# Kernel tuning notes

Hardware: AMD Instinct MI355X
Metric: run time of the kernel (lower is better)

The kernel has to match this reference:

```python
import jax, jax.numpy as jnp
import numpy as np

T, N, E = 512, 64, 1024   # encoder frames, batch, encoder feature dim
H = 320                   # pred_hidden_size
J = 512                   # joint hidden
V = 29                    # vocab incl. blank
BLANK = V - 1
MAX_SYM = 30              # max_symbols_per_step


def setup_inputs() -> dict:
    key = jax.random.key(0)
    ks = jax.random.split(key, 16)
    sH = 1.0 / np.sqrt(H)
    sE = 1.0 / np.sqrt(E)
    sJ = 1.0 / np.sqrt(J)
    b_o = jax.random.normal(ks[14], (V,), jnp.float32) * 0.1
    b_o = b_o.at[BLANK].add(4.0)  # blank-dominant logits -> realistic sparse emissions
    return {
        "f": jax.random.normal(ks[0], (T, N, E), jnp.float32),
        "f_lens": jax.random.randint(ks[1], (N,), T // 2, T + 1).astype(jnp.int32),
        "emb": jax.random.normal(ks[2], (V - 1, H), jnp.float32) * 0.1,
        "wi0": jax.random.normal(ks[3], (4 * H, H), jnp.float32) * sH,
        "wh0": jax.random.normal(ks[4], (4 * H, H), jnp.float32) * sH,
        "bi0": jax.random.normal(ks[5], (4 * H,), jnp.float32) * 0.05,
        "bh0": jax.random.normal(ks[6], (4 * H,), jnp.float32) * 0.05,
        "wi1": jax.random.normal(ks[7], (4 * H, H), jnp.float32) * sH,
        "wh1": jax.random.normal(ks[8], (4 * H, H), jnp.float32) * sH,
        "bi1": jax.random.normal(ks[9], (4 * H,), jnp.float32) * 0.05,
        "bh1": jax.random.normal(ks[10], (4 * H,), jnp.float32) * 0.05,
        "w_f": jax.random.normal(ks[11], (J, E), jnp.float32) * sE,
        "w_g": jax.random.normal(ks[12], (J, H), jnp.float32) * sH,
        "b_j": jax.random.normal(ks[13], (J,), jnp.float32) * 0.05,
        "w_o": jax.random.normal(ks[15], (V, J), jnp.float32) * sJ,
        "b_o": b_o,
    }


def reference(f, f_lens, emb, wi0, wh0, bi0, bh0, wi1, wh1, bi1, bh1,
              w_f, w_g, b_j, w_o, b_o):
    n = f.shape[1]
    rows = jnp.arange(n)

    def cell(x, h, c, wi, wh, bi, bh):
        g = x @ wi.T + h @ wh.T + (bi + bh)
        i, fg, gg, o = jnp.split(g, 4, axis=-1)  # torch LSTM gate order i,f,g,o
        c2 = jax.nn.sigmoid(fg) * c + jax.nn.sigmoid(i) * jnp.tanh(gg)
        return jax.nn.sigmoid(o) * jnp.tanh(c2), c2

    def pred_step(last_sym, h, c):
        # SOS (=-1) embeds to zeros
        x = jnp.where(last_sym[:, None] < 0, 0.0, emb[jnp.clip(last_sym, 0, V - 2)])
        h0, c0 = cell(x, h[0], c[0], wi0, wh0, bi0, bh0)
        h1, c1 = cell(h0, h[1], c[1], wi1, wh1, bi1, bh1)
        return h1, jnp.stack([h0, h1]), jnp.stack([c0, c1])

    def joint(fi, g):
        hj = jax.nn.relu(fi @ w_f.T + g @ w_g.T + b_j)
        return hj @ w_o.T + b_o

    def cond(st):
        return jnp.any(st[0] < f_lens)

    def body(st):
        time_idx, sym_add, res, res_idx, last, h, c = st
        fi = f[jnp.clip(time_idx, 0, T - 1), rows]            # [N,E] per-element frame
        g, h_new, c_new = pred_step(last, h, c)               # one LSTM step
        sym = jnp.argmax(joint(fi, g), axis=1).astype(jnp.int32)
        active = time_idx < f_lens
        emit = active & (sym != BLANK) & (sym_add < MAX_SYM)
        adv = active & ~emit                                   # blank or symbol cap -> advance time
        slot = jnp.where(emit, res_idx + 1, 0)
        res = res.at[rows, slot].set(jnp.where(emit, sym, res[rows, slot]))
        res_idx = res_idx + emit.astype(jnp.int32)
        sym_add = jnp.where(emit, sym_add + 1, jnp.where(adv, 0, sym_add))
        time_idx = time_idx + adv.astype(jnp.int32)
        last = jnp.where(emit, sym, last)
        m = emit[None, :, None]
        return (time_idx, sym_add, res, res_idx, last,
                jnp.where(m, h_new, h), jnp.where(m, c_new, c))

    init = (jnp.zeros((n,), jnp.int32),                        # time_idx
            jnp.zeros((n,), jnp.int32),                        # symbols_added
            jnp.full((n, MAX_SYM * T), -1, jnp.int32),         # res
            jnp.full((n,), -1, jnp.int32),                     # res_idx
            jnp.full((n,), -1, jnp.int32),                     # pred_g (SOS)
            jnp.zeros((2, n, H), jnp.float32),                 # pred h
            jnp.zeros((2, n, H), jnp.float32))                 # pred c
    st = jax.lax.while_loop(cond, body, init)
    res, res_idx = st[2], st[3]
    return res, res_idx + 1
```

## Files before the change

kernel.cpp:

```cpp
#include <hip/hip_runtime.h>
#include <math.h>

#define T_ 512
#define N_ 64
#define E_ 1024
#define H_ 320
#define HS8_ 40
#define J_ 512
#define V_ 29
#define BLANK_ 28
#define MAXSYM_ 30
#define RESW_ (MAXSYM_ * T_)

#define BM_ 128
#define BN_ 128
#define BK_ 16
#define GEMMB_ 1024

__device__ float g_Xi0[V_][4 * H_];
__device__ float g_b1s[4 * H_];
__device__ float g_h0x[2][N_][H_];
__device__ float g_h1x[2][N_][H_];
__device__ float g_gpx[2][N_][8][J_];
__device__ unsigned int g_flag[N_];

#define BSW_ 144
__device__ __forceinline__ int padcol(int c) { return c + ((c >> 5) << 2); }

__global__ __launch_bounds__(256) void gemm_init_kernel(
    const float* __restrict__ A, const float* __restrict__ B,
    const float* __restrict__ bj, float* __restrict__ C,
    const float* __restrict__ emb, const float* __restrict__ wi0,
    const float* __restrict__ bi0, const float* __restrict__ bh0,
    const float* __restrict__ bi1, const float* __restrict__ bh1,
    int* __restrict__ res) {
  const int bid = blockIdx.x;
  const int tid = threadIdx.x;

  if (bid >= GEMMB_) {
    const int ab = bid - GEMMB_;
    if (ab < V_) {
      __shared__ __align__(16) float xs[H_];
      for (int i = tid; i < H_; i += 256)
        xs[i] = (ab < V_ - 1) ? emb[(size_t)ab * H_ + i] : 0.f;
      __syncthreads();
      for (int o = tid; o < 4 * H_; o += 256) {
        float acc = bi0[o] + bh0[o];
        if (ab < V_ - 1) {
          const float* wr = wi0 + (size_t)o * H_;
          for (int k = 0; k < H_; k += 4) {
            float4 x4 = *(const float4*)&xs[k];
            float4 w4 = *(const float4*)&wr[k];
            acc += x4.x * w4.x + x4.y * w4.y + x4.z * w4.z + x4.w * w4.w;
          }
        }
        g_Xi0[ab][o] = acc;
        if (ab == 0) g_b1s[o] = bi1[o] + bh1[o];
      }
    } else {
      if (ab == V_ && tid < N_) g_flag[tid] = 0u;
      const int fb = ab - V_;
      int4* r4 = (int4*)res;
      const size_t tot = (size_t)N_ * RESW_ / 4;
      const size_t i0 = (size_t)fb * 256 + tid;
      const int4 mval = {-1, -1, -1, -1};
      for (size_t i = i0; i < tot; i += 3 * 256) r4[i] = mval;
    }
    return;
  }

  __shared__ __align__(16) float As[BK_][BM_ + 4];
  __shared__ __align__(16) float Bs[BK_][BSW_];
  const int m0 = blockIdx.x / 4 * BM_;
  const int j0 = (blockIdx.x & 3) * BN_;
  const int tx = tid & 15, ty = tid >> 4;
  const int sm = tid >> 1;
  const int sk = (tid & 1) << 3;
  const int smP = padcol(sm);
  const int bcol = padcol(tx * 8);

  float acc[8][8];
#pragma unroll
  for (int i = 0; i < 8; ++i)
#pragma unroll
    for (int j = 0; j < 8; ++j) acc[i][j] = 0.f;

  for (int kc = 0; kc < E_; kc += BK_) {
    float4 av0 = *(const float4*)(A + (size_t)(m0 + sm) * E_ + kc + sk);
    float4 av1 = *(const float4*)(A + (size_t)(m0 + sm) * E_ + kc + sk + 4);
    float4 bv0 = *(const float4*)(B + (size_t)(j0 + sm) * E_ + kc + sk);
    float4 bv1 = *(const float4*)(B + (size_t)(j0 + sm) * E_ + kc + sk + 4);
    __syncthreads();
    As[sk + 0][sm] = av0.x; As[sk + 1][sm] = av0.y;
    As[sk + 2][sm] = av0.z; As[sk + 3][sm] = av0.w;
    As[sk + 4][sm] = av1.x; As[sk + 5][sm] = av1.y;
    As[sk + 6][sm] = av1.z; As[sk + 7][sm] = av1.w;
    Bs[sk + 0][smP] = bv0.x; Bs[sk + 1][smP] = bv0.y;
    Bs[sk + 2][smP] = bv0.z; Bs[sk + 3][smP] = bv0.w;
    Bs[sk + 4][smP] = bv1.x; Bs[sk + 5][smP] = bv1.y;
    Bs[sk + 6][smP] = bv1.z; Bs[sk + 7][smP] = bv1.w;
    __syncthreads();
#pragma unroll
    for (int k = 0; k < BK_; ++k) {
      float a_[8], b_[8];
      *(float4*)&a_[0] = *(const float4*)&As[k][ty * 8];
      *(float4*)&a_[4] = *(const float4*)&As[k][ty * 8 + 4];
      *(float4*)&b_[0] = *(const float4*)&Bs[k][bcol];
      *(float4*)&b_[4] = *(const float4*)&Bs[k][bcol + 4];
#pragma unroll
      for (int i = 0; i < 8; ++i)
#pragma unroll
        for (int j = 0; j < 8; ++j) acc[i][j] += a_[i] * b_[j];
    }
  }

#pragma unroll
  for (int i = 0; i < 8; ++i) {
    const size_t m = (size_t)(m0 + ty * 8 + i);
#pragma unroll
    for (int j = 0; j < 8; j += 4) {
      float4 v;
      v.x = acc[i][j + 0] + bj[j0 + tx * 8 + j + 0];
      v.y = acc[i][j + 1] + bj[j0 + tx * 8 + j + 1];
      v.z = acc[i][j + 2] + bj[j0 + tx * 8 + j + 2];
      v.w = acc[i][j + 3] + bj[j0 + tx * 8 + j + 3];
      *(float4*)(C + m * J_ + j0 + tx * 8 + j) = v;
    }
  }
}

__device__ __forceinline__ float sigmoidf_(float x) {
  return 1.f / (1.f + expf(-x));
}

__device__ __forceinline__ void flag_round8(int row, int tid, int& target) {
  target += 8;
  __syncthreads();
  if (tid == 0) {
    __hip_atomic_fetch_add(&g_flag[row], 1u, __ATOMIC_RELEASE,
                           __HIP_MEMORY_SCOPE_AGENT);
    while (__hip_atomic_load(&g_flag[row], __ATOMIC_ACQUIRE,
                             __HIP_MEMORY_SCOPE_AGENT) < (unsigned)target)
      __builtin_amdgcn_s_sleep(1);
  }
  __syncthreads();
}

__device__ void recompute8(
    int s, int row, int k8, int tid, int par, int& target,
    const float* __restrict__ wh0, const float* __restrict__ wi1,
    const float* __restrict__ wh1, const float* __restrict__ w_g,
    float* h0s, float* h1s, float* gates,
    float& c0, float& c1, float2& gp) {
  const int g = tid / HS8_;
  const int il = tid - g * HS8_;
  const int o = g * H_ + k8 * HS8_ + il;

  if (tid < 4 * HS8_) {
    const float* wr = wh0 + (size_t)o * H_;
    float acc = g_Xi0[s][o];
    for (int kk = 0; kk < H_; kk += 4) {
      float4 h4 = *(const float4*)&h0s[kk];
      float4 w4 = *(const float4*)&wr[kk];
      acc += h4.x * w4.x + h4.y * w4.y + h4.z * w4.z + h4.w * w4.w;
    }
    gates[tid] = acc;
  }
  __syncthreads();
  if (tid < HS8_) {
    float ig = sigmoidf_(gates[tid]);
    float fg = sigmoidf_(gates[HS8_ + tid]);
    float gg = tanhf(gates[2 * HS8_ + tid]);
    float og = sigmoidf_(gates[3 * HS8_ + tid]);
    float c2 = fg * c0 + ig * gg;
    c0 = c2;
    float h2 = og * tanhf(c2);
    __hip_atomic_store(&g_h0x[par][row][k8 * HS8_ + tid], h2, __ATOMIC_RELAXED,
                       __HIP_MEMORY_SCOPE_AGENT);
  }
  float acc1 = 0.f;
  if (tid < 4 * HS8_) {
    const float* whr = wh1 + (size_t)o * H_;
    acc1 = g_b1s[o];
    for (int kk = 0; kk < H_; kk += 4) {
      float4 h4 = *(const float4*)&h1s[kk];
      float4 w4 = *(const float4*)&whr[kk];
      acc1 += h4.x * w4.x + h4.y * w4.y + h4.z * w4.z + h4.w * w4.w;
    }
  }
  flag_round8(row, tid, target);
  h0s[tid] = __hip_atomic_load(&g_h0x[par][row][tid], __ATOMIC_RELAXED,
                               __HIP_MEMORY_SCOPE_AGENT);
  if (tid < H_ - 256)
    h0s[256 + tid] = __hip_atomic_load(&g_h0x[par][row][256 + tid],
                                       __ATOMIC_RELAXED, __HIP_MEMORY_SCOPE_AGENT);
  __syncthreads();
  if (tid < 4 * HS8_) {
    const float* wir = wi1 + (size_t)o * H_;
    for (int kk = 0; kk < H_; kk += 4) {
      float4 x4 = *(const float4*)&h0s[kk];
      float4 w4 = *(const float4*)&wir[kk];
      acc1 += x4.x * w4.x + x4.y * w4.y + x4.z * w4.z + x4.w * w4.w;
    }
    gates[tid] = acc1;
  }
  __syncthreads();
  if (tid < HS8_) {
    float ig = sigmoidf_(gates[tid]);
    float fg = sigmoidf_(gates[HS8_ + tid]);
    float gg = tanhf(gates[2 * HS8_ + tid]);
    float og = sigmoidf_(gates[3 * HS8_ + tid]);
    float c2 = fg * c1 + ig * gg;
    c1 = c2;
    float h2 = og * tanhf(c2);
    h1s[k8 * HS8_ + tid] = h2;
    __hip_atomic_store(&g_h1x[par][row][k8 * HS8_ + tid], h2, __ATOMIC_RELAXED,
                       __HIP_MEMORY_SCOPE_AGENT);
  }
  __syncthreads();
  {
    const float* hsl = &h1s[k8 * HS8_];
#pragma unroll
    for (int jj = 0; jj < 2; ++jj) {
      const int j = tid + jj * 256;
      const float* wgr = w_g + (size_t)j * H_ + k8 * HS8_;
      float a = 0.f;
      for (int kk = 0; kk < HS8_; kk += 4) {
        float4 h4 = *(const float4*)&hsl[kk];
        float4 w4 = *(const float4*)&wgr[kk];
        a += h4.x * w4.x + h4.y * w4.y + h4.z * w4.z + h4.w * w4.w;
      }
      __hip_atomic_store(&g_gpx[par][row][k8][j], a, __ATOMIC_RELAXED,
                         __HIP_MEMORY_SCOPE_AGENT);
    }
  }
  flag_round8(row, tid, target);
  {
    float ax = 0.f, ay = 0.f;
#pragma unroll
    for (int kk = 0; kk < 8; ++kk) {
      ax += __hip_atomic_load(&g_gpx[par][row][kk][2 * tid], __ATOMIC_RELAXED,
                              __HIP_MEMORY_SCOPE_AGENT);
      ay += __hip_atomic_load(&g_gpx[par][row][kk][2 * tid + 1], __ATOMIC_RELAXED,
                              __HIP_MEMORY_SCOPE_AGENT);
    }
    gp.x = ax; gp.y = ay;
  }
  h1s[tid] = __hip_atomic_load(&g_h1x[par][row][tid], __ATOMIC_RELAXED,
                               __HIP_MEMORY_SCOPE_AGENT);
  if (tid < H_ - 256)
    h1s[256 + tid] = __hip_atomic_load(&g_h1x[par][row][256 + tid],
                                       __ATOMIC_RELAXED, __HIP_MEMORY_SCOPE_AGENT);
  __syncthreads();
}

__global__ __launch_bounds__(256, 2) void decode8(
    const float* __restrict__ Fproj, const int* __restrict__ f_lens,
    const float* __restrict__ wh0,
    const float* __restrict__ wi1, const float* __restrict__ wh1,
    const float* __restrict__ w_g,
    const float* __restrict__ w_o, const float* __restrict__ b_o,
    int* __restrict__ res, int* __restrict__ nsym) {
  const int bid = blockIdx.x;
  const int k8 = bid & 7;
  const int row = ((bid >> 3) + 8 * k8) & 63;
  const int tid = threadIdx.x;
  const int f_len = f_lens[row];

  __shared__ __align__(16) float h0s[H_], h1s[H_];
  __shared__ __align__(16) float gates[4 * HS8_];
  __shared__ __align__(16) float hjs[J_];
  __shared__ float logits[32];

  const int v = tid >> 3;
  const int lq = tid & 7;
  float4 wo[16];
  float bo = 0.f;
  if (v < V_) {
#pragma unroll
    for (int q = 0; q < 16; ++q)
      wo[q] = *(const float4*)(w_o + (size_t)v * J_ + lq * 4 + 32 * q);
    bo = b_o[v];
  }

  for (int i = tid; i < H_; i += 256) { h0s[i] = 0.f; h1s[i] = 0.f; }
  float c0 = 0.f, c1 = 0.f;
  float2 gp = {0.f, 0.f};
  int target = 0;
  __syncthreads();

  recompute8(BLANK_, row, k8, tid, 0, target, wh0, wi1, wh1, w_g,
             h0s, h1s, gates, c0, c1, gp);
  int ecount = 1;

  int t_loc = 0, sym_add = 0, res_idx = -1;
  float2 fp = *(const float2*)(Fproj + (size_t)row * J_ + 2 * tid);

  while (t_loc < f_len) {
    const int tn = (t_loc + 1 < T_) ? t_loc + 1 : T_ - 1;
    float2 fpn = *(const float2*)(Fproj + ((size_t)tn * N_ + row) * J_ + 2 * tid);

    float hx = fp.x + gp.x, hy = fp.y + gp.y;
    float2 hj2 = {hx > 0.f ? hx : 0.f, hy > 0.f ? hy : 0.f};
    *(float2*)&hjs[2 * tid] = hj2;
    __syncthreads();

    float p = 0.f;
    if (v < V_) {
#pragma unroll
      for (int q = 0; q < 16; ++q) {
        float4 h4 = *(const float4*)&hjs[lq * 4 + 32 * q];
        p += h4.x * wo[q].x + h4.y * wo[q].y + h4.z * wo[q].z + h4.w * wo[q].w;
      }
    }
    p += __shfl_xor(p, 4, 8);
    p += __shfl_xor(p, 2, 8);
    p += __shfl_xor(p, 1, 8);
    if (v < V_ && lq == 0) logits[v] = p + bo;
    __syncthreads();

    float best = logits[0];
    int bi = 0;
#pragma unroll
    for (int vv = 1; vv < V_; ++vv) {
      float lv = logits[vv];
      if (lv > best) { best = lv; bi = vv; }
    }
    const int emit = (bi != BLANK_) && (sym_add < MAXSYM_);

    if (emit) {
      res_idx += 1;
      if (k8 == 0 && tid == 0) res[(size_t)row * RESW_ + res_idx] = bi;
      sym_add += 1;
      recompute8(bi, row, k8, tid, ecount & 1, target, wh0, wi1, wh1, w_g,
                 h0s, h1s, gates, c0, c1, gp);
      ecount += 1;
    } else {
      sym_add = 0;
      t_loc += 1;
      fp = fpn;
    }
  }

  if (k8 == 0 && tid == 0) nsym[row] = res_idx + 1;
}

extern "C" void kernel_launch(void* const* d_in, const int* in_sizes, int n_in,
                              void* d_out, int out_size, void* d_ws, size_t ws_size,
                              hipStream_t stream) {
  const float* f      = (const float*)d_in[0];
  const int*   f_lens = (const int*)d_in[1];
  const float* emb    = (const float*)d_in[2];
  const float* wi0    = (const float*)d_in[3];
  const float* wh0    = (const float*)d_in[4];
  const float* bi0    = (const float*)d_in[5];
  const float* bh0    = (const float*)d_in[6];
  const float* wi1    = (const float*)d_in[7];
  const float* wh1    = (const float*)d_in[8];
  const float* bi1    = (const float*)d_in[9];
  const float* bh1    = (const float*)d_in[10];
  const float* w_f    = (const float*)d_in[11];
  const float* w_g    = (const float*)d_in[12];
  const float* b_j    = (const float*)d_in[13];
  const float* w_o    = (const float*)d_in[14];
  const float* b_o    = (const float*)d_in[15];

  int* out  = (int*)d_out;
  int* res  = out;
  int* nsym = out + (size_t)N_ * RESW_;

  float* Fproj = (float*)d_ws;

  gemm_init_kernel<<<GEMMB_ + 32, 256, 0, stream>>>(
      f, w_f, b_j, Fproj, emb, wi0, bi0, bh0, bi1, bh1, res);

  decode8<<<N_ * 8, 256, 0, stream>>>(Fproj, f_lens, wh0, wi1, wh1, w_g,
                                      w_o, b_o, res, nsym);
}
```

Baseline: 1.932 ms.

## Split each decode row across 16 cooperating blocks with split-K gate dot products

The per-row decode is spread over 16 blocks instead of 8. Each block now owns 20 hidden units, and two threads split each gate row's K dimension and combine their halves with a shuffle. This cuts the serial dot-product length per thread and the per-block weight traffic for each emitted symbol. In exchange the flag barrier waits on twice as many blocks, the partial-sum reduction over g_gpx doubles, and the launch needs 4 blocks per CU to stay co-resident. The spin-wait barrier can deadlock if not all 1024 blocks are resident at once.

Result: slower. 2.185 ms (+13.1%).

```diff
diff --git a/kernel.cpp b/kernel.cpp
--- a/kernel.cpp
+++ b/kernel.cpp
@@ -5,7 +5,7 @@
 #define N_ 64
 #define E_ 1024
 #define H_ 320
-#define HS8_ 40
+#define HS16_ 20
 #define J_ 512
 #define V_ 29
 #define BLANK_ 28
@@ -21,7 +21,7 @@
 __device__ float g_b1s[4 * H_];
 __device__ float g_h0x[2][N_][H_];
 __device__ float g_h1x[2][N_][H_];
-__device__ float g_gpx[2][N_][8][J_];
+__device__ float g_gpx[2][N_][16][J_];
 __device__ unsigned int g_flag[N_];
 
 #define BSW_ 144
@@ -133,8 +133,8 @@
   return 1.f / (1.f + expf(-x));
 }
 
-__device__ __forceinline__ void flag_round8(int row, int tid, int& target) {
-  target += 8;
+__device__ __forceinline__ void flag_round16(int row, int tid, int& target) {
+  target += 16;
   __syncthreads();
   if (tid == 0) {
     __hip_atomic_fetch_add(&g_flag[row], 1u, __ATOMIC_RELEASE,
@@ -146,99 +146,105 @@
   __syncthreads();
 }
 
-__device__ void recompute8(
-    int s, int row, int k8, int tid, int par, int& target,
+__device__ void recompute16(
+    int s, int row, int k16, int tid, int par, int& target,
     const float* __restrict__ wh0, const float* __restrict__ wi1,
     const float* __restrict__ wh1, const float* __restrict__ w_g,
     float* h0s, float* h1s, float* gates,
     float& c0, float& c1, float2& gp) {
-  const int g = tid / HS8_;
-  const int il = tid - g * HS8_;
-  const int o = g * H_ + k8 * HS8_ + il;
-
-  if (tid < 4 * HS8_) {
+  const int p = tid >> 1;
+  const int half = tid & 1;
+  const int g = p / HS16_;
+  const int il = p - g * HS16_;
+  const int o = g * H_ + k16 * HS16_ + il;
+  const int k0 = half * (H_ / 2);
+
+  if (p < 4 * HS16_) {
     const float* wr = wh0 + (size_t)o * H_;
-    float acc = g_Xi0[s][o];
-    for (int kk = 0; kk < H_; kk += 4) {
+    float acc = half ? 0.f : g_Xi0[s][o];
+    for (int kk = k0; kk < k0 + H_ / 2; kk += 4) {
       float4 h4 = *(const float4*)&h0s[kk];
       float4 w4 = *(const float4*)&wr[kk];
       acc += h4.x * w4.x + h4.y * w4.y + h4.z * w4.z + h4.w * w4.w;
     }
-    gates[tid] = acc;
-  }
-  __syncthreads();
-  if (tid < HS8_) {
+    acc += __shfl_xor(acc, 1, 2);
+    if (half == 0) gates[p] = acc;
+  }
+  __syncthreads();
+  if (tid < HS16_) {
     float ig = sigmoidf_(gates[tid]);
-    float fg = sigmoidf_(gates[HS8_ + tid]);
-    float gg = tanhf(gates[2 * HS8_ + tid]);
-    float og = sigmoidf_(gates[3 * HS8_ + tid]);
+    float fg = sigmoidf_(gates[HS16_ + tid]);
+    float gg = tanhf(gates[2 * HS16_ + tid]);
+    float og = sigmoidf_(gates[3 * HS16_ + tid]);
     float c2 = fg * c0 + ig * gg;
     c0 = c2;
     float h2 = og * tanhf(c2);
-    __hip_atomic_store(&g_h0x[par][row][k8 * HS8_ + tid], h2, __ATOMIC_RELAXED,
-                       __HIP_MEMORY_SCOPE_AGENT);
+    __hip_atomic_store(&g_h0x[par][row][k16 * HS16_ + tid], h2,
+                       __ATOMIC_RELAXED, __HIP_MEMORY_SCOPE_AGENT);
   }
   float acc1 = 0.f;
-  if (tid < 4 * HS8_) {
+  if (p < 4 * HS16_) {
     const float* whr = wh1 + (size_t)o * H_;
-    acc1 = g_b1s[o];
-    for (int kk = 0; kk < H_; kk += 4) {
+    acc1 = half ? 0.f : g_b1s[o];
+    for (int kk = k0; kk < k0 + H_ / 2; kk += 4) {
       float4 h4 = *(const float4*)&h1s[kk];
       float4 w4 = *(const float4*)&whr[kk];
       acc1 += h4.x * w4.x + h4.y * w4.y + h4.z * w4.z + h4.w * w4.w;
     }
   }
-  flag_round8(row, tid, target);
+  flag_round16(row, tid, target);
   h0s[tid] = __hip_atomic_load(&g_h0x[par][row][tid], __ATOMIC_RELAXED,
                                __HIP_MEMORY_SCOPE_AGENT);
   if (tid < H_ - 256)
     h0s[256 + tid] = __hip_atomic_load(&g_h0x[par][row][256 + tid],
                                        __ATOMIC_RELAXED, __HIP_MEMORY_SCOPE_AGENT);
   __syncthreads();
-  if (tid < 4 * HS8_) {
+  if (p < 4 * HS16_) {
     const float* wir = wi1 + (size_t)o * H_;
-    for (int kk = 0; kk < H_; kk += 4) {
+    for (int kk = k0; kk < k0 + H_ / 2; kk += 4) {
       float4 x4 = *(const float4*)&h0s[kk];
       float4 w4 = *(const float4*)&wir[kk];
       acc1 += x4.x * w4.x + x4.y * w4.y + x4.z * w4.z + x4.w * w4.w;
     }
-    gates[tid] = acc1;
-  }
-  __syncthreads();
-  if (tid < HS8_) {
+    acc1 += __shfl_xor(acc1, 1, 2);
+    if (half == 0) gates[p] = acc1;
+  }
+  __syncthreads();
+  if (tid < HS16_) {
     float ig = sigmoidf_(gates[tid]);
-    float fg = sigmoidf_(gates[HS8_ + tid]);
-    float gg = tanhf(gates[2 * HS8_ + tid]);
-    float og = sigmoidf_(gates[3 * HS8_ + tid]);
+    float fg = sigmoidf_(gates[HS16_ + tid]);
+    float gg = tanhf(gates[2 * HS16_ + tid]);
+    float og = sigmoidf_(gates[3 * HS16_ + tid]);
     float c2 = fg * c1 + ig * gg;
     c1 = c2;
     float h2 = og * tanhf(c2);
-    h1s[k8 * HS8_ + tid] = h2;
-    __hip_atomic_store(&g_h1x[par][row][k8 * HS8_ + tid], h2, __ATOMIC_RELAXED,
-                       __HIP_MEMORY_SCOPE_AGENT);
+    h1s[k16 * HS16_ + tid] = h2;
+    __hip_atomic_store(&g_h1x[par][row][k16 * HS16_ + tid], h2,
+                       __ATOMIC_RELAXED, __HIP_MEMORY_SCOPE_AGENT);
   }
   __syncthreads();
   {
-    const float* hsl = &h1s[k8 * HS8_];
+    const float* hsl = &h1s[k16 * HS16_];
 #pragma unroll
     for (int jj = 0; jj < 2; ++jj) {
       const int j = tid + jj * 256;
-      const float* wgr = w_g + (size_t)j * H_ + k8 * HS8_;
+      const float* wgr = w_g + (size_t)j * H_ + k16 * HS16_;
       float a = 0.f;
-      for (int kk = 0; kk < HS8_; kk += 4) {
+#pragma unroll
+      for (int kk = 0; kk < HS16_; kk += 4) {
         float4 h4 = *(const float4*)&hsl[kk];
         float4 w4 = *(const float4*)&wgr[kk];
         a += h4.x * w4.x + h4.y * w4.y + h4.z * w4.z + h4.w * w4.w;
       }
-      __hip_atomic_store(&g_gpx[par][row][k8][j], a, __ATOMIC_RELAXED,
+      __hip_atomic_store(&g_gpx[par][row][k16][j], a, __ATOMIC_RELAXED,
                          __HIP_MEMORY_SCOPE_AGENT);
     }
   }
-  flag_round8(row, tid, target);
+  flag_round16(row, tid, target);
   {
     float ax = 0.f, ay = 0.f;
 #pragma unroll
-    for (int kk = 0; kk < 8; ++kk) {
+    for (int kk = 0; kk < 16; ++kk) {
       ax += __hip_atomic_load(&g_gpx[par][row][kk][2 * tid], __ATOMIC_RELAXED,
                               __HIP_MEMORY_SCOPE_AGENT);
       ay += __hip_atomic_load(&g_gpx[par][row][kk][2 * tid + 1], __ATOMIC_RELAXED,
@@ -254,7 +260,7 @@
   __syncthreads();
 }
 
-__global__ __launch_bounds__(256, 2) void decode8(
+__global__ __launch_bounds__(256, 4) void decode16(
     const float* __restrict__ Fproj, const int* __restrict__ f_lens,
     const float* __restrict__ wh0,
     const float* __restrict__ wi1, const float* __restrict__ wh1,
@@ -262,13 +268,13 @@
     const float* __restrict__ w_o, const float* __restrict__ b_o,
     int* __restrict__ res, int* __restrict__ nsym) {
   const int bid = blockIdx.x;
-  const int k8 = bid & 7;
-  const int row = ((bid >> 3) + 8 * k8) & 63;
+  const int k16 = bid & 15;
+  const int row = ((bid >> 4) + 4 * k16) & 63;
   const int tid = threadIdx.x;
   const int f_len = f_lens[row];
 
   __shared__ __align__(16) float h0s[H_], h1s[H_];
-  __shared__ __align__(16) float gates[4 * HS8_];
+  __shared__ __align__(16) float gates[4 * HS16_];
   __shared__ __align__(16) float hjs[J_];
   __shared__ float logits[32];
 
@@ -289,8 +295,8 @@
   int target = 0;
   __syncthreads();
 
-  recompute8(BLANK_, row, k8, tid, 0, target, wh0, wi1, wh1, w_g,
-             h0s, h1s, gates, c0, c1, gp);
+  recompute16(BLANK_, row, k16, tid, 0, target, wh0, wi1, wh1, w_g,
+              h0s, h1s, gates, c0, c1, gp);
   int ecount = 1;
 
   int t_loc = 0, sym_add = 0, res_idx = -1;
@@ -330,10 +336,10 @@
 
     if (emit) {
       res_idx += 1;
-      if (k8 == 0 && tid == 0) res[(size_t)row * RESW_ + res_idx] = bi;
+      if (k16 == 0 && tid == 0) res[(size_t)row * RESW_ + res_idx] = bi;
       sym_add += 1;
-      recompute8(bi, row, k8, tid, ecount & 1, target, wh0, wi1, wh1, w_g,
-                 h0s, h1s, gates, c0, c1, gp);
+      recompute16(bi, row, k16, tid, ecount & 1, target, wh0, wi1, wh1, w_g,
+                  h0s, h1s, gates, c0, c1, gp);
       ecount += 1;
     } else {
       sym_add = 0;
@@ -342,7 +348,7 @@
     }
   }
 
-  if (k8 == 0 && tid == 0) nsym[row] = res_idx + 1;
+  if (k16 == 0 && tid == 0) nsym[row] = res_idx + 1;
 }
 
 extern "C" void kernel_launch(void* const* d_in, const int* in_sizes, int n_in,
@@ -374,6 +380,6 @@
   gemm_init_kernel<<<GEMMB_ + 32, 256, 0, stream>>>(
       f, w_f, b_j, Fproj, emb, wi0, bi0, bh0, bi1, bh1, res);
 
-  decode8<<<N_ * 8, 256, 0, stream>>>(Fproj, f_lens, wh0, wi1, wh1, w_g,
-                                      w_o, b_o, res, nsym);
-}
+  decode16<<<N_ * 16, 256, 0, stream>>>(Fproj, f_lens, wh0, wi1, wh1, w_g,
+                                        w_o, b_o, res, nsym);
+}
```
